# Optimization experiments

Hardware: AMD Instinct MI355X
Metric: run time of the kernel (lower is better)

## Reference

```python
import jax, jax.numpy as jnp
import numpy as np

N = 100000          # nodes
D_TEXT = 200        # text embedding dim
D_SEL = 2           # selector embedding dim (zero-padded in pos embs)
D = D_TEXT + D_SEL  # 202
E_TYPES = 6         # 3 forward edge types * 2 (backward edges)
M = 200000          # edges per edge type
N_POS = 512
SMALL_NUMBER = 1e-8


def position_embeddings(n_pos, demb, dpad):
    # Faithful to ProGraML PositionEmbeddings: sinusoid sin||cos, zero-padded.
    pos = jnp.arange(n_pos, dtype=jnp.float32)
    inv_freq = 1.0 / (10000.0 ** (jnp.arange(0, demb, 2, dtype=jnp.float32) / demb))
    sin_inp = pos[:, None] * inv_freq[None, :]                    # [n_pos, demb/2]
    emb = jnp.concatenate([jnp.sin(sin_inp), jnp.cos(sin_inp)], axis=-1)
    return jnp.concatenate([emb, jnp.zeros((n_pos, dpad), emb.dtype)], axis=1)  # [n_pos, demb+dpad]


def setup_inputs() -> dict:
    key = jax.random.key(0)
    ks = jax.random.split(key, 6)
    return {
        "node_states": jax.random.normal(ks[0], (N, D), jnp.float32),
        "edges": jax.random.randint(ks[1], (E_TYPES, M, 2), 0, N),      # [:, :, 0]=src, [:, :, 1]=tgt
        "pos_lists": jax.random.randint(ks[2], (E_TYPES, M), 0, N_POS),
        "W_transform": jax.random.normal(ks[3], (D, D * E_TYPES), jnp.float32) * 0.05,
        "b_transform": jnp.zeros((D * E_TYPES,), jnp.float32),
        "W_pos": jax.random.normal(ks[4], (D, D), jnp.float32) * 0.05,
        "b_pos": jnp.zeros((D,), jnp.float32),
    }


def reference(node_states, edges, pos_lists, W_transform, b_transform, W_pos, b_pos):
    # Positional gating: 2*sigmoid(Linear(position_embs))  -> [512, D]
    pos_embs = position_embeddings(N_POS, D_TEXT, D_SEL)
    pos_gating = 2.0 * jax.nn.sigmoid(pos_embs @ W_pos + b_pos)

    # Dense transform: [N, D] @ [D, E*D] -> view as [N, E, D]
    # (matches torch transpose(0,1).view(E, D, N) followed by per-type transpose back)
    prop = (node_states @ W_transform + b_transform).reshape(N, E_TYPES, D)

    src = edges[..., 0]  # [E, M]
    tgt = edges[..., 1]  # [E, M]

    # Per-edge-type gather of transformed source states: msgs[e, m] = prop[src[e, m], e]
    msgs = prop[src, jnp.arange(E_TYPES)[:, None], :]             # [E, M, D]
    msgs = msgs * pos_gating[pos_lists]                           # positional gate

    # Scatter-add over targets (all edge types fused into one segment_sum)
    flat_tgt = tgt.reshape(-1)
    summed = jax.ops.segment_sum(msgs.reshape(-1, D), flat_tgt, num_segments=N)  # [N, D]

    # Mean aggregation: bincount of targets, zeros treated as 1
    bincount = jax.ops.segment_sum(jnp.ones((E_TYPES * M,), jnp.float32), flat_tgt, num_segments=N)
    divisor = jnp.where(bincount == 0, 1.0, bincount) + SMALL_NUMBER
    return summed / divisor[:, None]
```

## Files before the change

kernel.cpp:

```cpp
#include <hip/hip_runtime.h>
#include <hip/hip_bf16.h>
#include <math.h>

#define NN   100000
#define NNP  100096
#define DD   202
#define ET   6
#define MM   200000
#define NE   (ET*MM)
#define NPOS 512
#define GDP  204
#define DE   1212
#define PDE  1216
#define KK   202
#define KP   224
#define NP   1280

typedef __attribute__((ext_vector_type(8))) short bf16x8;
typedef __attribute__((ext_vector_type(4))) float f32x4;

static __device__ inline unsigned short f2b(float f) {
    union { __hip_bfloat16 h; unsigned short s; } u;
    u.h = __float2bfloat16(f);
    return u.s;
}

static __device__ inline void glds16(const unsigned short* g, unsigned short* l) {
    __builtin_amdgcn_global_load_lds(
        (const __attribute__((address_space(1))) unsigned int*)g,
        (__attribute__((address_space(3))) unsigned int*)l, 16, 0, 0);
}

__global__ void gating_kernel(const float* __restrict__ W_pos,
                              const float* __restrict__ b_pos,
                              float* __restrict__ gating) {
    int p = blockIdx.x;
    __shared__ float emb[DD];
    int t = threadIdx.x;
    if (t < 100) {
        float invf = expf(-((float)t / 100.0f) * 9.210340371976184f);
        float si = (float)p * invf;
        emb[t]       = sinf(si);
        emb[100 + t] = cosf(si);
    } else if (t < 102) {
        emb[100 + t] = 0.0f;
    }
    __syncthreads();
    if (t < GDP) {
        float g = 0.0f;
        if (t < DD) {
            float acc = b_pos[t];
            for (int k = 0; k < DD; ++k) acc += emb[k] * W_pos[k * DD + t];
            g = 2.0f / (1.0f + expf(-acc));
        }
        gating[p * GDP + t] = g;
    }
}

__global__ void convB_kernel(const float* __restrict__ W, unsigned short* __restrict__ Bt) {
    int id = blockIdx.x * 256 + threadIdx.x;
    if (id >= NP * KP) return;
    int n = id / KP, k = id % KP;
    float v = (k < KK && n < DE) ? W[(size_t)k * DE + n] : 0.0f;
    Bt[id] = f2b(v);
}

__global__ void convA_kernel(const float* __restrict__ A, unsigned short* __restrict__ Abf) {
    int id = blockIdx.x * 256 + threadIdx.x;
    if (id >= NNP * (KP / 2)) return;
    int row = id / (KP / 2), kp = (id % (KP / 2)) * 2;
    float2 v = make_float2(0.0f, 0.0f);
    if (row < NN && kp < KK) v = *(const float2*)&A[(size_t)row * KK + kp];
    ushort2 o; o.x = f2b(v.x); o.y = f2b(v.y);
    *(ushort2*)&Abf[(size_t)row * KP + kp] = o;
}

__global__ __launch_bounds__(256) void gemm_mfma(const unsigned short* __restrict__ Abf,
                                                 const unsigned short* __restrict__ Bt,
                                                 const float* __restrict__ bias,
                                                 unsigned short* __restrict__ C) {
    __shared__ unsigned short sA[4096];
    __shared__ unsigned short sB[4096];
    __shared__ unsigned short sE[4608];
    int t    = threadIdx.x;
    int lane = t & 63;
    int wave = t >> 6;
    int q    = lane >> 4;
    int r16  = lane & 15;
    int wm   = (wave >> 1) * 64;
    int wn   = (wave & 1) * 64;
    int row0 = blockIdx.y * 128;
    int col0 = blockIdx.x * 128;

    int lrow = lane >> 2;
    int gch  = (lane & 3) ^ ((lrow >> 1) & 3);
    const unsigned short* aS0 = Abf + (size_t)(row0 + wave * 32 + lrow) * KP + gch * 8;
    const unsigned short* aS1 = aS0 + 16 * KP;
    const unsigned short* bS0 = Bt  + (size_t)(col0 + wave * 32 + lrow) * KP + gch * 8;
    const unsigned short* bS1 = bS0 + 16 * KP;
    unsigned short* lA0 = &sA[(wave * 32) * 32];
    unsigned short* lA1 = &sA[(wave * 32 + 16) * 32];
    unsigned short* lB0 = &sB[(wave * 32) * 32];
    unsigned short* lB1 = &sB[(wave * 32 + 16) * 32];

    f32x4 acc[4][4] = {};
    int swzr = (r16 >> 1) & 3;

    for (int kc = 0; kc < KP; kc += 32) {
        glds16(aS0 + kc, lA0);
        glds16(aS1 + kc, lA1);
        glds16(bS0 + kc, lB0);
        glds16(bS1 + kc, lB1);
        __syncthreads();

        bf16x8 a[4], b[4];
        #pragma unroll
        for (int mi = 0; mi < 4; ++mi)
            a[mi] = *(const bf16x8*)&sA[(wm + mi * 16 + r16) * 32 + (q ^ swzr) * 8];
        #pragma unroll
        for (int ni = 0; ni < 4; ++ni)
            b[ni] = *(const bf16x8*)&sB[(wn + ni * 16 + r16) * 32 + (q ^ swzr) * 8];
        #pragma unroll
        for (int mi = 0; mi < 4; ++mi)
            #pragma unroll
            for (int ni = 0; ni < 4; ++ni)
                acc[mi][ni] = __builtin_amdgcn_mfma_f32_16x16x32_bf16(a[mi], b[ni], acc[mi][ni], 0, 0, 0);
        __syncthreads();
    }

    float bb[4];
    #pragma unroll
    for (int ni = 0; ni < 4; ++ni) {
        int col = col0 + wn + ni * 16 + r16;
        bb[ni] = (col < DE) ? bias[col] : 0.0f;
    }
    int epi = wave * 1152;
    int rl = lane >> 3, ck = lane & 7;
    #pragma unroll
    for (int mi = 0; mi < 4; ++mi) {
        #pragma unroll
        for (int ni = 0; ni < 4; ++ni)
            #pragma unroll
            for (int ri = 0; ri < 4; ++ri)
                sE[epi + (q * 4 + ri) * 72 + ni * 16 + r16] = f2b(acc[mi][ni][ri] + bb[ni]);
        #pragma unroll
        for (int ii = 0; ii < 2; ++ii) {
            int rr = ii * 8 + rl;
            bf16x8 v = *(const bf16x8*)&sE[epi + rr * 72 + ck * 8];
            int grow = row0 + wm + mi * 16 + rr;
            int gcol = col0 + wn + ck * 8;
            if (grow < NN && gcol < PDE)
                *(bf16x8*)&C[(size_t)grow * PDE + gcol] = v;
        }
    }
}

__global__ __launch_bounds__(256) void count_kernel(const int* __restrict__ edges,
                                                    int* __restrict__ count) {
    int i = blockIdx.x * 256 + threadIdx.x;
    if (i >= NE) return;
    atomicAdd(&count[edges[2 * i + 1]], 1);
}

__global__ __launch_bounds__(256) void alloc_kernel(const int* __restrict__ count,
                                                    int* __restrict__ start,
                                                    int* __restrict__ cursor) {
    int t = blockIdx.x * 256 + threadIdx.x;
    int c = (t < NN) ? count[t] : 0;
    __shared__ int s[256];
    __shared__ int base;
    s[threadIdx.x] = c;
    __syncthreads();
    int v = c;
    for (int off = 1; off < 256; off <<= 1) {
        int u = (threadIdx.x >= off) ? s[threadIdx.x - off] : 0;
        __syncthreads();
        v += u;
        s[threadIdx.x] = v;
        __syncthreads();
    }
    if (threadIdx.x == 255) base = atomicAdd(cursor, v);
    __syncthreads();
    if (t < NN) start[t] = base + v - c;
}

__global__ __launch_bounds__(256) void scatter_kernel(const int* __restrict__ edges,
                                                      const int* __restrict__ pos_lists,
                                                      int* __restrict__ start,
                                                      unsigned* __restrict__ recs) {
    int i = blockIdx.x * 256 + threadIdx.x;
    if (i >= NE) return;
    int2 st = *(const int2*)&edges[2 * i];
    int e = (int)((unsigned)i / MM);
    unsigned rec = (unsigned)st.x | ((unsigned)e << 17) | ((unsigned)pos_lists[i] << 20);
    int p = atomicAdd(&start[st.y], 1);
    recs[p] = rec;
}

__global__ __launch_bounds__(256) void gather_kernel(const unsigned short* __restrict__ prop,
                                                     const float* __restrict__ gating,
                                                     const int* __restrict__ count,
                                                     const int* __restrict__ seg_end,
                                                     const unsigned* __restrict__ recs,
                                                     float* __restrict__ out) {
    int wid = blockIdx.x * 4 + (threadIdx.x >> 6);
    if (wid >= NN) return;
    int lane = threadIdx.x & 63;
    int c = count[wid];
    int end = seg_end[wid];
    int begin = end - c;
    int d = lane * 4;
    bool act = d < DD;
    float a0 = 0.f, a1 = 0.f, a2 = 0.f, a3 = 0.f;

    for (int base = begin; base < end; base += 64) {
        int n = end - base; if (n > 64) n = 64;
        unsigned rec = 0u;
        if (lane < n) rec = recs[base + lane];
        int poff = (int)(rec & 0x1FFFFu) * PDE + (int)((rec >> 17) & 7u) * DD;
        int goff = (int)(rec >> 20) * GDP;

        for (int jj = 0; jj < n; jj += 4) {
            int po[4], go[4];
            #pragma unroll
            for (int u = 0; u < 4; ++u) {
                int j = jj + u; if (j >= n) j = jj;
                po[u] = __shfl(poff, j);
                go[u] = __shfl(goff, j);
            }
            uint2  pv[4];
            float4 gv[4];
            #pragma unroll
            for (int u = 0; u < 4; ++u) {
                pv[u] = make_uint2(0u, 0u);
                gv[u] = make_float4(0.f, 0.f, 0.f, 0.f);
                if (act) {
                    pv[u] = *(const uint2*)&prop[po[u] + d];
                    gv[u] = *(const float4*)&gating[go[u] + d];
                }
            }
            __builtin_amdgcn_sched_barrier(0);
            #pragma unroll
            for (int u = 0; u < 4; ++u) {
                if (jj + u < n || u == 0) {
                    a0 += __uint_as_float(pv[u].x << 16)         * gv[u].x;
                    a1 += __uint_as_float(pv[u].x & 0xffff0000u) * gv[u].y;
                    a2 += __uint_as_float(pv[u].y << 16)         * gv[u].z;
                    a3 += __uint_as_float(pv[u].y & 0xffff0000u) * gv[u].w;
                }
            }
        }
    }

    float div = (c == 0 ? 1.0f : (float)c) + 1e-8f;
    float inv = 1.0f / div;
    if (act) {
        float* orow = out + (size_t)wid * DD;
        *(float2*)&orow[d] = make_float2(a0 * inv, a1 * inv);
        if (d + 2 < DD) *(float2*)&orow[d + 2] = make_float2(a2 * inv, a3 * inv);
    }
}

extern "C" void kernel_launch(void* const* d_in, const int* in_sizes, int n_in,
                              void* d_out, int out_size, void* d_ws, size_t ws_size,
                              hipStream_t stream) {
    const float* node_states = (const float*)d_in[0];
    const int*   edges       = (const int*)d_in[1];
    const int*   pos_lists   = (const int*)d_in[2];
    const float* W_transform = (const float*)d_in[3];
    const float* b_transform = (const float*)d_in[4];
    const float* W_pos       = (const float*)d_in[5];
    const float* b_pos       = (const float*)d_in[6];
    float* out = (float*)d_out;

    float* gating   = (float*)d_ws;
    int*   count    = (int*)(gating + NPOS * GDP);
    int*   start    = count + NN;
    int*   cursor   = start + NN;
    unsigned short* Bt  = (unsigned short*)(cursor + 4);
    unsigned short* Abf = Bt + NP * KP;
    unsigned* recs  = (unsigned*)(Abf + (size_t)NNP * KP);
    unsigned short* prop = (unsigned short*)(recs + NE);

    hipMemsetAsync(count, 0, NN * sizeof(int), stream);
    hipMemsetAsync(cursor, 0, sizeof(int), stream);

    gating_kernel<<<NPOS, 256, 0, stream>>>(W_pos, b_pos, gating);
    convB_kernel<<<(NP * KP + 255) / 256, 256, 0, stream>>>(W_transform, Bt);
    convA_kernel<<<(NNP * (KP / 2) + 255) / 256, 256, 0, stream>>>(node_states, Abf);

    dim3 g2(NP / 128, NNP / 128);
    gemm_mfma<<<g2, 256, 0, stream>>>(Abf, Bt, b_transform, prop);

    count_kernel<<<(NE + 255) / 256, 256, 0, stream>>>(edges, count);
    alloc_kernel<<<(NN + 255) / 256, 256, 0, stream>>>(count, start, cursor);
    scatter_kernel<<<(NE + 255) / 256, 256, 0, stream>>>(edges, pos_lists, start, recs);
    gather_kernel<<<(NN + 3) / 4, 256, 0, stream>>>(prop, gating, count, start, recs, out);
}
```

Before: 648.3 us.

## Double-buffer gather loads through LDS and store gating table in fp16

The gather kernel now issues per-edge prop and gating row loads straight into per-wave LDS double buffers with global_load_lds, and uses manual vmcnt waits so the next group's loads overlap with accumulating the current group. The gating table is stored as fp16 with a 256-element stride, which halves its bytes and aligns rows for 4-byte LDS loads. This trades register-held loads for LDS traffic plus explicit waitcnt scheduling. It also reads past the 202-element rows (512 bytes per row), and fp16 gating adds small precision loss.

```diff
diff --git a/kernel.cpp b/kernel.cpp
--- a/kernel.cpp
+++ b/kernel.cpp
@@ -1,5 +1,6 @@
 #include <hip/hip_runtime.h>
 #include <hip/hip_bf16.h>
+#include <hip/hip_fp16.h>
 #include <math.h>
 
 #define NN   100000
@@ -9,13 +10,16 @@
 #define MM   200000
 #define NE   (ET*MM)
 #define NPOS 512
-#define GDP  204
+#define GDP  256
 #define DE   1212
 #define PDE  1216
 #define KK   202
 #define KP   224
 #define NP   1280
 
+#define EG   4
+#define SLOT 1024
+
 typedef __attribute__((ext_vector_type(8))) short bf16x8;
 typedef __attribute__((ext_vector_type(4))) float f32x4;
 
@@ -31,9 +35,15 @@
         (__attribute__((address_space(3))) unsigned int*)l, 16, 0, 0);
 }
 
+static __device__ inline void glds4(const void* g, void* l) {
+    __builtin_amdgcn_global_load_lds(
+        (const __attribute__((address_space(1))) unsigned int*)g,
+        (__attribute__((address_space(3))) unsigned int*)l, 4, 0, 0);
+}
+
 __global__ void gating_kernel(const float* __restrict__ W_pos,
                               const float* __restrict__ b_pos,
-                              float* __restrict__ gating) {
+                              unsigned short* __restrict__ gat) {
     int p = blockIdx.x;
     __shared__ float emb[DD];
     int t = threadIdx.x;
@@ -53,7 +63,9 @@
             for (int k = 0; k < DD; ++k) acc += emb[k] * W_pos[k * DD + t];
             g = 2.0f / (1.0f + expf(-acc));
         }
-        gating[p * GDP + t] = g;
+        union { __half h; unsigned short s; } u;
+        u.h = __float2half_rn(g);
+        gat[p * GDP + t] = u.s;
     }
 }
 
@@ -197,58 +209,83 @@
     recs[p] = rec;
 }
 
+
+#define VMW16 do { asm volatile("s_waitcnt vmcnt(16)" ::: "memory"); \
+                   __builtin_amdgcn_sched_barrier(0); } while (0)
+#define VMW0  do { asm volatile("s_waitcnt vmcnt(0)"  ::: "memory"); \
+                   __builtin_amdgcn_sched_barrier(0); } while (0)
+#define LKW0  do { asm volatile("s_waitcnt lgkmcnt(0)" ::: "memory"); \
+                   __builtin_amdgcn_sched_barrier(0); } while (0)
+
+#define ISSUE(G)                                                          \
+  {                                                                       \
+    LKW0;     \
+    char* slot_ = wlds + (((G) & 1) * (EG * SLOT));                       \
+    _Pragma("unroll")                                                     \
+    for (int u_ = 0; u_ < EG; ++u_) {                                     \
+      int j_ = (G) * EG + u_; if (j_ >= n) j_ = n - 1;                    \
+      int pb_ = __builtin_amdgcn_readlane(pby, j_);                       \
+      int gb_ = __builtin_amdgcn_readlane(gby, j_);                       \
+      char* sl_ = slot_ + u_ * SLOT;                                      \
+      glds4(prop8 + pb_ +       lane * 4, sl_);                           \
+      glds4(prop8 + pb_ + 256 + lane * 4, sl_ + 256);                     \
+      glds4(gat8  + gb_ +       lane * 4, sl_ + 512);                     \
+      glds4(gat8  + gb_ + 256 + lane * 4, sl_ + 768);                     \
+    }                                                                     \
+  }
+
+#define CONSUME(G)                                                        \
+  {                                                                       \
+    char* slot_ = wlds + (((G) & 1) * (EG * SLOT));                       \
+    _Pragma("unroll")                                                     \
+    for (int u_ = 0; u_ < EG; ++u_) {                                     \
+      if ((G) * EG + u_ < n) {                                            \
+        uint2 pv_ = *(const uint2*)(slot_ + u_ * SLOT + dd2);             \
+        uint2 gv_ = *(const uint2*)(slot_ + u_ * SLOT + 512 + dd2);       \
+        float2 g01_ = __half22float2(*(const __half2*)&gv_.x);            \
+        float2 g23_ = __half22float2(*(const __half2*)&gv_.y);            \
+        a0 += __uint_as_float(pv_.x << 16)         * g01_.x;              \
+        a1 += __uint_as_float(pv_.x & 0xffff0000u) * g01_.y;              \
+        a2 += __uint_as_float(pv_.y << 16)         * g23_.x;              \
+        a3 += __uint_as_float(pv_.y & 0xffff0000u) * g23_.y;              \
+      }                                                                   \
+    }                                                                     \
+  }
+
 __global__ __launch_bounds__(256) void gather_kernel(const unsigned short* __restrict__ prop,
-                                                     const float* __restrict__ gating,
+                                                     const unsigned short* __restrict__ gat,
                                                      const int* __restrict__ count,
                                                      const int* __restrict__ seg_end,
                                                      const unsigned* __restrict__ recs,
                                                      float* __restrict__ out) {
-    int wid = blockIdx.x * 4 + (threadIdx.x >> 6);
+    __shared__ __align__(16) char lds[4 * 2 * EG * SLOT];
+    int wave = threadIdx.x >> 6;
+    int lane = threadIdx.x & 63;
+    char* wlds = &lds[wave * (2 * EG * SLOT)];
+    int wid = blockIdx.x * 4 + wave;
     if (wid >= NN) return;
-    int lane = threadIdx.x & 63;
     int c = count[wid];
     int end = seg_end[wid];
     int begin = end - c;
     int d = lane * 4;
     bool act = d < DD;
+    int dd2 = d * 2;
+    const char* prop8 = (const char*)prop;
+    const char* gat8  = (const char*)gat;
     float a0 = 0.f, a1 = 0.f, a2 = 0.f, a3 = 0.f;
 
     for (int base = begin; base < end; base += 64) {
         int n = end - base; if (n > 64) n = 64;
         unsigned rec = 0u;
         if (lane < n) rec = recs[base + lane];
-        int poff = (int)(rec & 0x1FFFFu) * PDE + (int)((rec >> 17) & 7u) * DD;
-        int goff = (int)(rec >> 20) * GDP;
-
-        for (int jj = 0; jj < n; jj += 4) {
-            int po[4], go[4];
-            #pragma unroll
-            for (int u = 0; u < 4; ++u) {
-                int j = jj + u; if (j >= n) j = jj;
-                po[u] = __shfl(poff, j);
-                go[u] = __shfl(goff, j);
-            }
-            uint2  pv[4];
-            float4 gv[4];
-            #pragma unroll
-            for (int u = 0; u < 4; ++u) {
-                pv[u] = make_uint2(0u, 0u);
-                gv[u] = make_float4(0.f, 0.f, 0.f, 0.f);
-                if (act) {
-                    pv[u] = *(const uint2*)&prop[po[u] + d];
-                    gv[u] = *(const float4*)&gating[go[u] + d];
-                }
-            }
-            __builtin_amdgcn_sched_barrier(0);
-            #pragma unroll
-            for (int u = 0; u < 4; ++u) {
-                if (jj + u < n || u == 0) {
-                    a0 += __uint_as_float(pv[u].x << 16)         * gv[u].x;
-                    a1 += __uint_as_float(pv[u].x & 0xffff0000u) * gv[u].y;
-                    a2 += __uint_as_float(pv[u].y << 16)         * gv[u].z;
-                    a3 += __uint_as_float(pv[u].y & 0xffff0000u) * gv[u].w;
-                }
-            }
+        int pby = ((int)(rec & 0x1FFFFu) * PDE + (int)((rec >> 17) & 7u) * DD) * 2;
+        int gby = (int)(rec >> 20) << 9;
+
+        int ng = (n + EG - 1) >> 2;
+        ISSUE(0);
+        for (int g = 0; g < ng; ++g) {
+            if (g + 1 < ng) { ISSUE(g + 1); VMW16; } else { VMW0; }
+            CONSUME(g);
         }
     }
 
@@ -273,19 +310,20 @@
     const float* b_pos       = (const float*)d_in[6];
     float* out = (float*)d_out;
 
-    float* gating   = (float*)d_ws;
-    int*   count    = (int*)(gating + NPOS * GDP);
-    int*   start    = count + NN;
-    int*   cursor   = start + NN;
-    unsigned short* Bt  = (unsigned short*)(cursor + 4);
-    unsigned short* Abf = Bt + NP * KP;
-    unsigned* recs  = (unsigned*)(Abf + (size_t)NNP * KP);
-    unsigned short* prop = (unsigned short*)(recs + NE);
+    char* ws = (char*)d_ws;
+    unsigned short* gat = (unsigned short*)ws;  ws += (size_t)NPOS * GDP * 2;
+    int* count  = (int*)ws;                     ws += (size_t)NN * 4;
+    int* start  = (int*)ws;                     ws += (size_t)NN * 4;
+    int* cursor = (int*)ws;                     ws += 16;
+    unsigned short* Bt  = (unsigned short*)ws;  ws += (size_t)NP * KP * 2;
+    unsigned short* Abf = (unsigned short*)ws;  ws += (size_t)NNP * KP * 2;
+    unsigned* recs = (unsigned*)ws;             ws += (size_t)NE * 4;
+    unsigned short* prop = (unsigned short*)ws;
 
     hipMemsetAsync(count, 0, NN * sizeof(int), stream);
     hipMemsetAsync(cursor, 0, sizeof(int), stream);
 
-    gating_kernel<<<NPOS, 256, 0, stream>>>(W_pos, b_pos, gating);
+    gating_kernel<<<NPOS, 256, 0, stream>>>(W_pos, b_pos, gat);
     convB_kernel<<<(NP * KP + 255) / 256, 256, 0, stream>>>(W_transform, Bt);
     convA_kernel<<<(NNP * (KP / 2) + 255) / 256, 256, 0, stream>>>(node_states, Abf);
 
@@ -295,5 +333,5 @@
     count_kernel<<<(NE + 255) / 256, 256, 0, stream>>>(edges, count);
     alloc_kernel<<<(NN + 255) / 256, 256, 0, stream>>>(count, start, cursor);
     scatter_kernel<<<(NE + 255) / 256, 256, 0, stream>>>(edges, pos_lists, start, recs);
-    gather_kernel<<<(NN + 3) / 4, 256, 0, stream>>>(prop, gating, count, start, recs, out);
-}
+    gather_kernel<<<(NN + 3) / 4, 256, 0, stream>>>(prop, gat, count, start, recs, out);
+}
```

Result: no change. 657.0 us (+1.3%).

## Double-buffer GEMM LDS loads and store positional gating table in fp16

Applied to the files above, without the earlier changes.

The GEMM k-loop now prefetches the next 32-wide K chunk into a second LDS buffer while the current one runs through MFMA, using explicit vmcnt waits and raw barriers in place of __syncthreads. The epilogue scratch is aliased onto the same LDS array. Separately, the gating table is stored as fp16, halving the bytes the gather kernel loads per edge, and the sched_barrier in the gather loop is removed. In exchange, the gating values carry fp16 rounding error, and the hand-written waitcnt synchronisation is easier to get wrong.

```diff
diff --git a/kernel.cpp b/kernel.cpp
--- a/kernel.cpp
+++ b/kernel.cpp
@@ -1,5 +1,6 @@
 #include <hip/hip_runtime.h>
 #include <hip/hip_bf16.h>
+#include <hip/hip_fp16.h>
 #include <math.h>
 
 #define NN   100000
@@ -33,7 +34,7 @@
 
 __global__ void gating_kernel(const float* __restrict__ W_pos,
                               const float* __restrict__ b_pos,
-                              float* __restrict__ gating) {
+                              unsigned short* __restrict__ gat) {
     int p = blockIdx.x;
     __shared__ float emb[DD];
     int t = threadIdx.x;
@@ -53,7 +54,9 @@
             for (int k = 0; k < DD; ++k) acc += emb[k] * W_pos[k * DD + t];
             g = 2.0f / (1.0f + expf(-acc));
         }
-        gating[p * GDP + t] = g;
+        union { __half h; unsigned short s; } u;
+        u.h = __float2half_rn(g);
+        gat[p * GDP + t] = u.s;
     }
 }
 
@@ -79,9 +82,11 @@
                                                  const unsigned short* __restrict__ Bt,
                                                  const float* __restrict__ bias,
                                                  unsigned short* __restrict__ C) {
-    __shared__ unsigned short sA[4096];
-    __shared__ unsigned short sB[4096];
-    __shared__ unsigned short sE[4608];
+    __shared__ unsigned short lds[16384];
+    unsigned short* sA = lds;
+    unsigned short* sB = lds + 8192;
+    unsigned short* sE = lds;
+
     int t    = threadIdx.x;
     int lane = t & 63;
     int wave = t >> 6;
@@ -98,35 +103,45 @@
     const unsigned short* aS1 = aS0 + 16 * KP;
     const unsigned short* bS0 = Bt  + (size_t)(col0 + wave * 32 + lrow) * KP + gch * 8;
     const unsigned short* bS1 = bS0 + 16 * KP;
-    unsigned short* lA0 = &sA[(wave * 32) * 32];
-    unsigned short* lA1 = &sA[(wave * 32 + 16) * 32];
-    unsigned short* lB0 = &sB[(wave * 32) * 32];
-    unsigned short* lB1 = &sB[(wave * 32 + 16) * 32];
+
+#define STAGE(b, kc) do {                                   \
+        glds16(aS0 + (kc), &sA[(b)*4096 + wave*1024]);      \
+        glds16(aS1 + (kc), &sA[(b)*4096 + wave*1024+512]);  \
+        glds16(bS0 + (kc), &sB[(b)*4096 + wave*1024]);      \
+        glds16(bS1 + (kc), &sB[(b)*4096 + wave*1024+512]);  \
+    } while (0)
 
     f32x4 acc[4][4] = {};
     int swzr = (r16 >> 1) & 3;
 
-    for (int kc = 0; kc < KP; kc += 32) {
-        glds16(aS0 + kc, lA0);
-        glds16(aS1 + kc, lA1);
-        glds16(bS0 + kc, lB0);
-        glds16(bS1 + kc, lB1);
-        __syncthreads();
+    STAGE(0, 0);
+    for (int k = 0; k < 7; ++k) {
+        int cur = k & 1;
+        if (k < 6) {
+            STAGE(cur ^ 1, (k + 1) * 32);
+            asm volatile("s_waitcnt vmcnt(4)" ::: "memory");
+        } else {
+            asm volatile("s_waitcnt vmcnt(0)" ::: "memory");
+        }
+        __builtin_amdgcn_s_barrier();
 
         bf16x8 a[4], b[4];
+        int sbase = cur * 4096;
         #pragma unroll
         for (int mi = 0; mi < 4; ++mi)
-            a[mi] = *(const bf16x8*)&sA[(wm + mi * 16 + r16) * 32 + (q ^ swzr) * 8];
+            a[mi] = *(const bf16x8*)&sA[sbase + (wm + mi * 16 + r16) * 32 + (q ^ swzr) * 8];
         #pragma unroll
         for (int ni = 0; ni < 4; ++ni)
-            b[ni] = *(const bf16x8*)&sB[(wn + ni * 16 + r16) * 32 + (q ^ swzr) * 8];
+            b[ni] = *(const bf16x8*)&sB[sbase + (wn + ni * 16 + r16) * 32 + (q ^ swzr) * 8];
         #pragma unroll
         for (int mi = 0; mi < 4; ++mi)
             #pragma unroll
             for (int ni = 0; ni < 4; ++ni)
                 acc[mi][ni] = __builtin_amdgcn_mfma_f32_16x16x32_bf16(a[mi], b[ni], acc[mi][ni], 0, 0, 0);
-        __syncthreads();
-    }
+
+        __builtin_amdgcn_s_barrier();
+    }
+#undef STAGE
 
     float bb[4];
     #pragma unroll
@@ -198,7 +213,7 @@
 }
 
 __global__ __launch_bounds__(256) void gather_kernel(const unsigned short* __restrict__ prop,
-                                                     const float* __restrict__ gating,
+                                                     const unsigned short* __restrict__ gat,
                                                      const int* __restrict__ count,
                                                      const int* __restrict__ seg_end,
                                                      const unsigned* __restrict__ recs,
@@ -228,25 +243,25 @@
                 po[u] = __shfl(poff, j);
                 go[u] = __shfl(goff, j);
             }
-            uint2  pv[4];
-            float4 gv[4];
+            uint2 pv[4], gv[4];
             #pragma unroll
             for (int u = 0; u < 4; ++u) {
                 pv[u] = make_uint2(0u, 0u);
-                gv[u] = make_float4(0.f, 0.f, 0.f, 0.f);
+                gv[u] = make_uint2(0u, 0u);
                 if (act) {
                     pv[u] = *(const uint2*)&prop[po[u] + d];
-                    gv[u] = *(const float4*)&gating[go[u] + d];
+                    gv[u] = *(const uint2*)&gat[go[u] + d];
                 }
             }
-            __builtin_amdgcn_sched_barrier(0);
             #pragma unroll
             for (int u = 0; u < 4; ++u) {
                 if (jj + u < n || u == 0) {
-                    a0 += __uint_as_float(pv[u].x << 16)         * gv[u].x;
-                    a1 += __uint_as_float(pv[u].x & 0xffff0000u) * gv[u].y;
-                    a2 += __uint_as_float(pv[u].y << 16)         * gv[u].z;
-                    a3 += __uint_as_float(pv[u].y & 0xffff0000u) * gv[u].w;
+                    float2 g01 = __half22float2(*(const __half2*)&gv[u].x);
+                    float2 g23 = __half22float2(*(const __half2*)&gv[u].y);
+                    a0 += __uint_as_float(pv[u].x << 16)         * g01.x;
+                    a1 += __uint_as_float(pv[u].x & 0xffff0000u) * g01.y;
+                    a2 += __uint_as_float(pv[u].y << 16)         * g23.x;
+                    a3 += __uint_as_float(pv[u].y & 0xffff0000u) * g23.y;
                 }
             }
         }
@@ -273,19 +288,20 @@
     const float* b_pos       = (const float*)d_in[6];
     float* out = (float*)d_out;
 
-    float* gating   = (float*)d_ws;
-    int*   count    = (int*)(gating + NPOS * GDP);
-    int*   start    = count + NN;
-    int*   cursor   = start + NN;
-    unsigned short* Bt  = (unsigned short*)(cursor + 4);
-    unsigned short* Abf = Bt + NP * KP;
-    unsigned* recs  = (unsigned*)(Abf + (size_t)NNP * KP);
-    unsigned short* prop = (unsigned short*)(recs + NE);
+    char* ws = (char*)d_ws;
+    unsigned short* gat = (unsigned short*)ws;  ws += (size_t)NPOS * GDP * 2;
+    int* count  = (int*)ws;                     ws += (size_t)NN * 4;
+    int* start  = (int*)ws;                     ws += (size_t)NN * 4;
+    int* cursor = (int*)ws;                     ws += 16;
+    unsigned short* Bt  = (unsigned short*)ws;  ws += (size_t)NP * KP * 2;
+    unsigned short* Abf = (unsigned short*)ws;  ws += (size_t)NNP * KP * 2;
+    unsigned* recs = (unsigned*)ws;             ws += (size_t)NE * 4;
+    unsigned short* prop = (unsigned short*)ws;
 
     hipMemsetAsync(count, 0, NN * sizeof(int), stream);
     hipMemsetAsync(cursor, 0, sizeof(int), stream);
 
-    gating_kernel<<<NPOS, 256, 0, stream>>>(W_pos, b_pos, gating);
+    gating_kernel<<<NPOS, 256, 0, stream>>>(W_pos, b_pos, gat);
     convB_kernel<<<(NP * KP + 255) / 256, 256, 0, stream>>>(W_transform, Bt);
     convA_kernel<<<(NNP * (KP / 2) + 255) / 256, 256, 0, stream>>>(node_states, Abf);
 
@@ -295,5 +311,5 @@
     count_kernel<<<(NE + 255) / 256, 256, 0, stream>>>(edges, count);
     alloc_kernel<<<(NN + 255) / 256, 256, 0, stream>>>(count, start, cursor);
     scatter_kernel<<<(NE + 255) / 256, 256, 0, stream>>>(edges, pos_lists, start, recs);
-    gather_kernel<<<(NN + 3) / 4, 256, 0, stream>>>(prop, gating, count, start, recs, out);
-}
+    gather_kernel<<<(NN + 3) / 4, 256, 0, stream>>>(prop, gat, count, start, recs, out);
+}
```

Result: faster. 631.8 us (-2.5%).
